# Performance work log

Hardware: AMD Instinct MI355X
Metric: run time of the kernel (lower is better)

The kernel has to match this reference:

```python
import jax, jax.numpy as jnp
import numpy as np

N = 8192      # nodes
E = 262144    # edges (avg degree 32)
D_IN = 128    # feat dim (out_channels)
D_H = 256     # hidden_channels * 2
D_OUT = 64    # in_channels (final embedding dim)


def _sage_pool(feat, src, dst, n, Wp, bp, Ws, Wn, b, ew):
    # DGL SAGEConv('pool'): h_pool = relu(fc_pool(feat)); msg = h_pool[src] * ew;
    # h_neigh = max over in-edges (0 for isolated nodes);
    # out = fc_self(feat) + fc_neigh(h_neigh) + bias
    h = jax.nn.relu(feat @ Wp + bp)                          # [N, d_in]
    msg = h[src] * ew[:, None]                               # [E, d_in]
    agg = jax.ops.segment_max(msg, dst, num_segments=n)      # [N, d_in], -inf if no in-edges
    agg = jnp.where(jnp.isfinite(agg), agg, 0.0)
    return feat @ Ws + agg @ Wn + b


def setup_inputs() -> dict:
    key = jax.random.key(0)
    ks = jax.random.split(key, 20)
    feat = jax.random.normal(ks[0], (N, D_IN), dtype=jnp.float32)
    src = jax.random.randint(ks[1], (E,), 0, N)
    dst = jax.random.randint(ks[2], (E,), 0, N)
    edge_weight = jax.random.uniform(ks[3], (E,), dtype=jnp.float32)

    def lin(k, din, dout):
        return jax.random.normal(k, (din, dout), dtype=jnp.float32) / np.float32(np.sqrt(din))

    params = {}
    dims = [(D_IN, D_H), (D_H, D_H), (D_H, D_OUT)]
    i = 4
    for l, (di, do) in enumerate(dims, 1):
        params[f"Wp{l}"] = lin(ks[i], di, di); i += 1
        params[f"bp{l}"] = jnp.zeros((di,), jnp.float32)
        params[f"Ws{l}"] = lin(ks[i], di, do); i += 1
        params[f"Wn{l}"] = lin(ks[i], di, do); i += 1
        params[f"b{l}"] = jnp.zeros((do,), jnp.float32)

    return dict(feat=feat, src=src, dst=dst, edge_weight=edge_weight, n_nodes=N, **params)


def reference(feat, src, dst, edge_weight, n_nodes,
              Wp1, bp1, Ws1, Wn1, b1,
              Wp2, bp2, Ws2, Wn2, b2,
              Wp3, bp3, Ws3, Wn3, b3):
    hd = jax.nn.relu(_sage_pool(feat, src, dst, n_nodes, Wp1, bp1, Ws1, Wn1, b1, edge_weight))
    hd = jax.nn.relu(_sage_pool(hd,   src, dst, n_nodes, Wp2, bp2, Ws2, Wn2, b2, edge_weight))
    hd = jax.nn.relu(_sage_pool(hd,   src, dst, n_nodes, Wp3, bp3, Ws3, Wn3, b3, edge_weight))
    adj_rec = hd @ hd.T                                      # [N, N]
    return hd, adj_rec
```

## Files before the change

kernel.cpp:

```cpp
#include <hip/hip_runtime.h>
#include <hip/hip_bf16.h>

#define NN 8192
#define NE 262144
#define CAP 96

typedef __attribute__((ext_vector_type(8))) __bf16 bf16x8;
typedef __attribute__((ext_vector_type(4))) float f32x4;

__device__ __forceinline__ ushort f2b(float v) {
    __hip_bfloat16 b = __float2bfloat16(v);
    return *reinterpret_cast<ushort*>(&b);
}
__device__ __forceinline__ uint pack2(float lo, float hi) {
    return (uint)f2b(lo) | ((uint)f2b(hi) << 16);
}

struct PrepArgs {
    const float* feat; ushort* featb; int* cnt;
    const float* w[9]; ushort* wt[9];
};

__global__ __launch_bounds__(256) void prep_k(PrepArgs a) {
    const int bid = blockIdx.x, tid = threadIdx.x;
    if (bid < 32) {
        a.cnt[bid * 256 + tid] = 0;
        return;
    }
    if (bid < 32 + 1024) {
        int i = ((bid - 32) * 256 + tid) * 4;
        float4 f = *(const float4*)&a.feat[i];
        uint2 o; o.x = pack2(f.x, f.y); o.y = pack2(f.z, f.w);
        *(uint2*)&a.featb[i] = o;
        return;
    }
    int id = (bid - 1056) * 256 + tid;
    if (id >= 376832) return;
    const int cum[10] = {0, 16384, 49152, 81920, 147456, 212992, 278528, 344064, 360448, 376832};
    const int KK[9] = {128, 128, 128, 256, 256, 256, 256, 256, 256};
    const int LN[9] = {7, 8, 8, 8, 8, 8, 8, 6, 6};
    int m = 0;
#pragma unroll
    for (int t = 1; t < 9; ++t) m += (id >= cum[t]);
    int local = id - cum[m];
    int K = KK[m], ln = LN[m];
    int k = local >> ln, n = local & ((1 << ln) - 1);
    a.wt[m][n * K + k] = f2b(a.w[m][local]);
}

__global__ void scatter_direct_k(const int* __restrict__ src, const int* __restrict__ dst,
                                 const float* __restrict__ ew, int* __restrict__ cnt,
                                 uint2* __restrict__ slots) {
    int e = blockIdx.x * blockDim.x + threadIdx.x;
    if (e < NE) {
        int d = dst[e];
        int p = atomicAdd(&cnt[d], 1);
        if (p < CAP) slots[(size_t)d * CAP + p] = make_uint2((uint)src[e], __float_as_uint(ew[e]));
    }
}

#define AW2 72

template <int BM, int BN, bool DUAL, bool RELU, int OUTMODE>
__global__ __launch_bounds__(256, 4) void gemm_k(
    const ushort* __restrict__ A1, const ushort* __restrict__ BT1, int K1,
    const ushort* __restrict__ A2, const ushort* __restrict__ BT2, int K2,
    const float* __restrict__ bias, float* __restrict__ Cf,
    ushort* __restrict__ Cb, int N) {
    constexpr int MI = BM / 32, NJ = BN / 32;
    __shared__ __align__(16) ushort As[BM * AW2];
    __shared__ __align__(16) ushort Bs[BN * AW2];

    int tid = threadIdx.x;
    int lane = tid & 63, wave = tid >> 6;
    int wm = (wave >> 1) * (BM / 2), wn = (wave & 1) * (BN / 2);
    int r16 = lane & 15, kb = lane >> 4;
    int m0 = blockIdx.y * BM, n0 = blockIdx.x * BN;

    f32x4 acc[MI][NJ];
#pragma unroll
    for (int i = 0; i < MI; ++i)
#pragma unroll
        for (int j = 0; j < NJ; ++j) acc[i][j] = (f32x4)(0.f);

#pragma unroll 1
    for (int pass = 0; pass < (DUAL ? 2 : 1); ++pass) {
        const ushort* A = pass ? A2 : A1;
        const ushort* BT = pass ? BT2 : BT1;
        int K = pass ? K2 : K1;
        for (int k0 = 0; k0 < K; k0 += 64) {
#pragma unroll
            for (int rep = 0; rep < BM / 32; ++rep) {
                int id = rep * 256 + tid;
                int row = id >> 3, c = id & 7;
                *(bf16x8*)&As[row * AW2 + c * 8] =
                    *(const bf16x8*)&A[(size_t)(m0 + row) * K + k0 + c * 8];
            }
#pragma unroll
            for (int rep = 0; rep < BN / 32; ++rep) {
                int id = rep * 256 + tid;
                int row = id >> 3, c = id & 7;
                *(bf16x8*)&Bs[row * AW2 + c * 8] =
                    *(const bf16x8*)&BT[(size_t)(n0 + row) * K + k0 + c * 8];
            }
            __syncthreads();
#pragma unroll
            for (int kc = 0; kc < 2; ++kc) {
                bf16x8 a[MI], b[NJ];
#pragma unroll
                for (int i = 0; i < MI; ++i)
                    a[i] = *(const bf16x8*)&As[(wm + 16 * i + r16) * AW2 + kc * 32 + kb * 8];
#pragma unroll
                for (int j = 0; j < NJ; ++j)
                    b[j] = *(const bf16x8*)&Bs[(wn + 16 * j + r16) * AW2 + kc * 32 + kb * 8];
#pragma unroll
                for (int i = 0; i < MI; ++i)
#pragma unroll
                    for (int j = 0; j < NJ; ++j)
                        acc[i][j] = __builtin_amdgcn_mfma_f32_16x16x32_bf16(a[i], b[j], acc[i][j], 0, 0, 0);
            }
            __syncthreads();
        }
    }

#pragma unroll
    for (int i = 0; i < MI; ++i) {
#pragma unroll
        for (int j = 0; j < NJ; ++j) {
            int col = n0 + wn + 16 * j + r16;
            float bv = bias[col];
#pragma unroll
            for (int r = 0; r < 4; ++r) {
                int row = m0 + wm + 16 * i + kb * 4 + r;
                float v = acc[i][j][r] + bv;
                if (RELU) v = fmaxf(v, 0.f);
                if (OUTMODE != 0) Cf[(size_t)row * N + col] = v;
                if (OUTMODE != 1) Cb[(size_t)row * N + col] = f2b(v);
            }
        }
    }
}

template <int D>
__global__ __launch_bounds__(256) void seg_max_k4(
    const ushort* __restrict__ h, const int* __restrict__ cnt,
    const uint2* __restrict__ slots, ushort* __restrict__ agg) {
    constexpr int FPL = D / 64;
    int wave = threadIdx.x >> 6, lane = threadIdx.x & 63;
    int node = blockIdx.x * 4 + wave;
    int f0 = lane * FPL;
    int n = cnt[node];
    if (n > CAP) n = CAP;
    const uint2* sl = &slots[(size_t)node * CAP];
    float mx[FPL];
#pragma unroll
    for (int i = 0; i < FPL; ++i) mx[i] = 0.f;

    auto upd = [&](uint s, float w) {
        const uint* hp = (const uint*)&h[(size_t)s * D + f0];
#pragma unroll
        for (int c = 0; c < FPL / 2; ++c) {
            uint u = hp[c];
            float lo = __uint_as_float(u << 16);
            float hi = __uint_as_float(u & 0xffff0000u);
            mx[2 * c] = fmaxf(mx[2 * c], lo * w);
            mx[2 * c + 1] = fmaxf(mx[2 * c + 1], hi * w);
        }
    };

    int e = 0;
    for (; e + 8 <= n; e += 8) {
        uint2 d[8];
#pragma unroll
        for (int t = 0; t < 8; ++t) d[t] = sl[e + t];
#pragma unroll
        for (int t = 0; t < 8; ++t) upd(d[t].x, __uint_as_float(d[t].y));
    }
    for (; e < n; ++e) {
        uint2 d = sl[e];
        upd(d.x, __uint_as_float(d.y));
    }

    uint* ap = (uint*)&agg[(size_t)node * D + f0];
#pragma unroll
    for (int c = 0; c < FPL / 2; ++c) ap[c] = pack2(mx[2 * c], mx[2 * c + 1]);
}

__global__ __launch_bounds__(256) void aat_k(const ushort* __restrict__ H,
                                             float* __restrict__ C) {
    __shared__ __align__(16) ushort As[128 * 72];
    __shared__ __align__(16) ushort Bs[128 * 72];
    int tid = threadIdx.x, lane = tid & 63, wave = tid >> 6;
    int wm = (wave >> 1) * 64, wn = (wave & 1) * 64;
    int r16 = lane & 15, kb = lane >> 4;
    int m0 = blockIdx.y * 128, n0 = blockIdx.x * 128;

#pragma unroll
    for (int rep = 0; rep < 4; ++rep) {
        int id = rep * 256 + tid;
        int row = id >> 3, c = id & 7;
        *(bf16x8*)&As[row * 72 + c * 8] = *(const bf16x8*)&H[(size_t)(m0 + row) * 64 + c * 8];
        *(bf16x8*)&Bs[row * 72 + c * 8] = *(const bf16x8*)&H[(size_t)(n0 + row) * 64 + c * 8];
    }
    __syncthreads();

    f32x4 acc[4][4];
#pragma unroll
    for (int i = 0; i < 4; ++i)
#pragma unroll
        for (int j = 0; j < 4; ++j) acc[i][j] = (f32x4)(0.f);

#pragma unroll
    for (int kc = 0; kc < 2; ++kc) {
        bf16x8 a[4], b[4];
#pragma unroll
        for (int i = 0; i < 4; ++i)
            a[i] = *(const bf16x8*)&As[(wm + 16 * i + r16) * 72 + kc * 32 + kb * 8];
#pragma unroll
        for (int j = 0; j < 4; ++j)
            b[j] = *(const bf16x8*)&Bs[(wn + 16 * j + r16) * 72 + kc * 32 + kb * 8];
#pragma unroll
        for (int i = 0; i < 4; ++i)
#pragma unroll
            for (int j = 0; j < 4; ++j)
                acc[i][j] = __builtin_amdgcn_mfma_f32_16x16x32_bf16(a[i], b[j], acc[i][j], 0, 0, 0);
    }

#pragma unroll
    for (int i = 0; i < 4; ++i) {
#pragma unroll
        for (int j = 0; j < 4; ++j) {
            int col = n0 + wn + 16 * j + r16;
#pragma unroll
            for (int r = 0; r < 4; ++r) {
                size_t row = m0 + wm + 16 * i + kb * 4 + r;
                C[row * NN + col] = acc[i][j][r];
            }
        }
    }
}

extern "C" void kernel_launch(void* const* d_in, const int* in_sizes, int n_in,
                              void* d_out, int out_size, void* d_ws, size_t ws_size,
                              hipStream_t stream) {
    const float* feat = (const float*)d_in[0];
    const int* src = (const int*)d_in[1];
    const int* dst = (const int*)d_in[2];
    const float* ew = (const float*)d_in[3];
    const float* Wp1 = (const float*)d_in[5];
    const float* bp1 = (const float*)d_in[6];
    const float* Ws1 = (const float*)d_in[7];
    const float* Wn1 = (const float*)d_in[8];
    const float* b1  = (const float*)d_in[9];
    const float* Wp2 = (const float*)d_in[10];
    const float* bp2 = (const float*)d_in[11];
    const float* Ws2 = (const float*)d_in[12];
    const float* Wn2 = (const float*)d_in[13];
    const float* b2  = (const float*)d_in[14];
    const float* Wp3 = (const float*)d_in[15];
    const float* bp3 = (const float*)d_in[16];
    const float* Ws3 = (const float*)d_in[17];
    const float* Wn3 = (const float*)d_in[18];
    const float* b3  = (const float*)d_in[19];

    float* out = (float*)d_out;
    float* adj = out + (size_t)NN * 64;

    char* ws = (char*)d_ws;
    int* cnt      = (int*)(ws + 0x0);
    uint2* slots  = (uint2*)(ws + 0x10000);
    ushort* featb = (ushort*)(ws + 0x620000);
    ushort* Wp1T = (ushort*)(ws + 0x820000);
    ushort* Ws1T = (ushort*)(ws + 0x828000);
    ushort* Wn1T = (ushort*)(ws + 0x838000);
    ushort* Wp2T = (ushort*)(ws + 0x848000);
    ushort* Ws2T = (ushort*)(ws + 0x868000);
    ushort* Wn2T = (ushort*)(ws + 0x888000);
    ushort* Wp3T = (ushort*)(ws + 0x8A8000);
    ushort* Ws3T = (ushort*)(ws + 0x8C8000);
    ushort* Wn3T = (ushort*)(ws + 0x8D0000);
    ushort* P = (ushort*)(ws + 0x900000);
    ushort* G = (ushort*)(ws + 0xD00000);
    ushort* X = (ushort*)(ws + 0x1100000);
    ushort* Y = (ushort*)(ws + 0x1500000);
    ushort* hdb = (ushort*)(ws + 0x1900000);

    PrepArgs pa;
    pa.feat = feat; pa.featb = featb; pa.cnt = cnt;
    const float* wsrc[9] = {Wp1, Ws1, Wn1, Wp2, Ws2, Wn2, Wp3, Ws3, Wn3};
    ushort* wdst[9] = {Wp1T, Ws1T, Wn1T, Wp2T, Ws2T, Wn2T, Wp3T, Ws3T, Wn3T};
    for (int i = 0; i < 9; ++i) { pa.w[i] = wsrc[i]; pa.wt[i] = wdst[i]; }
    prep_k<<<32 + 1024 + 1472, 256, 0, stream>>>(pa);

    scatter_direct_k<<<NE / 256, 256, 0, stream>>>(src, dst, ew, cnt, slots);

    gemm_k<64, 64, false, true, 0><<<dim3(2, 128), 256, 0, stream>>>(
        featb, Wp1T, 128, nullptr, nullptr, 0, bp1, nullptr, P, 128);
    seg_max_k4<128><<<NN / 4, 256, 0, stream>>>(P, cnt, slots, G);
    gemm_k<64, 64, true, true, 0><<<dim3(4, 128), 256, 0, stream>>>(
        featb, Ws1T, 128, G, Wn1T, 128, b1, nullptr, X, 256);

    gemm_k<64, 64, false, true, 0><<<dim3(4, 128), 256, 0, stream>>>(
        X, Wp2T, 256, nullptr, nullptr, 0, bp2, nullptr, P, 256);
    seg_max_k4<256><<<NN / 4, 256, 0, stream>>>(P, cnt, slots, G);
    gemm_k<64, 64, true, true, 0><<<dim3(4, 128), 256, 0, stream>>>(
        X, Ws2T, 256, G, Wn2T, 256, b2, nullptr, Y, 256);

    gemm_k<64, 64, false, true, 0><<<dim3(4, 128), 256, 0, stream>>>(
        Y, Wp3T, 256, nullptr, nullptr, 0, bp3, nullptr, P, 256);
    seg_max_k4<256><<<NN / 4, 256, 0, stream>>>(P, cnt, slots, G);
    gemm_k<32, 64, true, true, 2><<<dim3(1, 256), 256, 0, stream>>>(
        Y, Ws3T, 256, G, Wn3T, 256, b3, out, hdb, 64);

    aat_k<<<dim3(NN / 128, NN / 128), 256, 0, stream>>>(hdb, adj);
}
```

Measured before the change: 166.5 us.

## Fuse segment-max, self/neigh GEMMs and next-layer pool GEMM per layer

Replaces the separate pool GEMM, segment-max and dual GEMM launches with one per-layer kernel. Each block gathers the max-aggregated neighbour features for 32 nodes into shared memory, runs the self and neighbour GEMMs, and then computes the next layer's pool projection from the tile held in shared memory. The layer-1 pool GEMM also moves into the scatter kernel, and feat is converted to bf16 inside the GEMM loads instead of in a separate pass. This removes several launches and the global round trips of G and P, but the 32-row tiles with only 256 blocks mean lower occupancy, and the atomic scatter and pool1 blocks in one grid can run concurrently. That is a correctness risk: layer_k reads cnt and slots only in a later launch, so it is probably fine.

```diff
diff --git a/kernel.cpp b/kernel.cpp
--- a/kernel.cpp
+++ b/kernel.cpp
@@ -17,24 +17,14 @@
 }
 
 struct PrepArgs {
-    const float* feat; ushort* featb; int* cnt;
+    int* cnt;
     const float* w[9]; ushort* wt[9];
 };
 
 __global__ __launch_bounds__(256) void prep_k(PrepArgs a) {
     const int bid = blockIdx.x, tid = threadIdx.x;
-    if (bid < 32) {
-        a.cnt[bid * 256 + tid] = 0;
-        return;
-    }
-    if (bid < 32 + 1024) {
-        int i = ((bid - 32) * 256 + tid) * 4;
-        float4 f = *(const float4*)&a.feat[i];
-        uint2 o; o.x = pack2(f.x, f.y); o.y = pack2(f.z, f.w);
-        *(uint2*)&a.featb[i] = o;
-        return;
-    }
-    int id = (bid - 1056) * 256 + tid;
+    if (bid < 32) { a.cnt[bid * 256 + tid] = 0; return; }
+    int id = (bid - 32) * 256 + tid;
     if (id >= 376832) return;
     const int cum[10] = {0, 16384, 49152, 81920, 147456, 212992, 278528, 344064, 360448, 376832};
     const int KK[9] = {128, 128, 128, 256, 256, 256, 256, 256, 256};
@@ -48,142 +38,236 @@
     a.wt[m][n * K + k] = f2b(a.w[m][local]);
 }
 
-__global__ void scatter_direct_k(const int* __restrict__ src, const int* __restrict__ dst,
-                                 const float* __restrict__ ew, int* __restrict__ cnt,
-                                 uint2* __restrict__ slots) {
-    int e = blockIdx.x * blockDim.x + threadIdx.x;
-    if (e < NE) {
+__global__ __launch_bounds__(256) void scat_pool1_k(
+    const int* __restrict__ src, const int* __restrict__ dst,
+    const float* __restrict__ ew, int* __restrict__ cnt, uint2* __restrict__ slots,
+    const float* __restrict__ feat, const ushort* __restrict__ WpT,
+    const float* __restrict__ bp, ushort* __restrict__ Pout) {
+    const int tid = threadIdx.x;
+    if (blockIdx.x < NE / 256) {
+        int e = blockIdx.x * 256 + tid;
         int d = dst[e];
         int p = atomicAdd(&cnt[d], 1);
         if (p < CAP) slots[(size_t)d * CAP + p] = make_uint2((uint)src[e], __float_as_uint(ew[e]));
-    }
-}
-
-#define AW2 72
-
-template <int BM, int BN, bool DUAL, bool RELU, int OUTMODE>
-__global__ __launch_bounds__(256, 4) void gemm_k(
-    const ushort* __restrict__ A1, const ushort* __restrict__ BT1, int K1,
-    const ushort* __restrict__ A2, const ushort* __restrict__ BT2, int K2,
-    const float* __restrict__ bias, float* __restrict__ Cf,
-    ushort* __restrict__ Cb, int N) {
-    constexpr int MI = BM / 32, NJ = BN / 32;
-    __shared__ __align__(16) ushort As[BM * AW2];
-    __shared__ __align__(16) ushort Bs[BN * AW2];
-
-    int tid = threadIdx.x;
-    int lane = tid & 63, wave = tid >> 6;
-    int wm = (wave >> 1) * (BM / 2), wn = (wave & 1) * (BN / 2);
-    int r16 = lane & 15, kb = lane >> 4;
-    int m0 = blockIdx.y * BM, n0 = blockIdx.x * BN;
-
-    f32x4 acc[MI][NJ];
-#pragma unroll
-    for (int i = 0; i < MI; ++i)
-#pragma unroll
-        for (int j = 0; j < NJ; ++j) acc[i][j] = (f32x4)(0.f);
-
-#pragma unroll 1
-    for (int pass = 0; pass < (DUAL ? 2 : 1); ++pass) {
-        const ushort* A = pass ? A2 : A1;
-        const ushort* BT = pass ? BT2 : BT1;
-        int K = pass ? K2 : K1;
-        for (int k0 = 0; k0 < K; k0 += 64) {
-#pragma unroll
-            for (int rep = 0; rep < BM / 32; ++rep) {
+        return;
+    }
+    __shared__ __align__(16) ushort As[32 * 72];
+    __shared__ __align__(16) ushort Bs[128 * 72];
+    const int m0 = (blockIdx.x - NE / 256) * 32;
+    const int lane = tid & 63, wave = tid >> 6;
+    const int r16 = lane & 15, kb = lane >> 4;
+    const int wm = (wave >> 1) * 16, wn = (wave & 1) * 64;
+
+    f32x4 acc[4];
+#pragma unroll
+    for (int j = 0; j < 4; ++j) acc[j] = (f32x4)(0.f);
+
+#pragma unroll
+    for (int k0 = 0; k0 < 128; k0 += 64) {
+#pragma unroll
+        for (int rep = 0; rep < 2; ++rep) {
+            int id = rep * 256 + tid;
+            int row = id >> 4, c = id & 15;
+            float4 f = *(const float4*)&feat[(size_t)(m0 + row) * 128 + k0 + c * 4];
+            uint2 o; o.x = pack2(f.x, f.y); o.y = pack2(f.z, f.w);
+            *(uint2*)&As[row * 72 + c * 4] = o;
+        }
+#pragma unroll
+        for (int rep = 0; rep < 4; ++rep) {
+            int id = rep * 256 + tid;
+            int row = id >> 3, c = id & 7;
+            *(bf16x8*)&Bs[row * 72 + c * 8] = *(const bf16x8*)&WpT[(size_t)row * 128 + k0 + c * 8];
+        }
+        __syncthreads();
+#pragma unroll
+        for (int kc = 0; kc < 2; ++kc) {
+            bf16x8 a = *(const bf16x8*)&As[(wm + r16) * 72 + kc * 32 + kb * 8];
+#pragma unroll
+            for (int j = 0; j < 4; ++j) {
+                bf16x8 b = *(const bf16x8*)&Bs[(wn + 16 * j + r16) * 72 + kc * 32 + kb * 8];
+                acc[j] = __builtin_amdgcn_mfma_f32_16x16x32_bf16(a, b, acc[j], 0, 0, 0);
+            }
+        }
+        __syncthreads();
+    }
+#pragma unroll
+    for (int j = 0; j < 4; ++j) {
+        int col = wn + 16 * j + r16;
+        float bv = bp[col];
+#pragma unroll
+        for (int rr = 0; rr < 4; ++rr) {
+            int rl = wm + kb * 4 + rr;
+            Pout[(size_t)(m0 + rl) * 128 + col] = f2b(fmaxf(acc[j][rr] + bv, 0.f));
+        }
+    }
+}
+
+template <int DIN, int DOUT, bool A1F32, bool POOL, bool LAST>
+__global__ __launch_bounds__(256) void layer_k(
+    const void* __restrict__ A1v, const ushort* __restrict__ Pin,
+    const int* __restrict__ cnt, const uint2* __restrict__ slots,
+    const ushort* __restrict__ WsT, const ushort* __restrict__ WnT,
+    const float* __restrict__ bias,
+    const ushort* __restrict__ WpT, const float* __restrict__ biasp,
+    ushort* __restrict__ Xout, float* __restrict__ Fout, ushort* __restrict__ Pout) {
+    constexpr int SG = DIN + 8, ST = DOUT + 8, NJ = DOUT / 32, FPL = DIN / 64;
+    __shared__ __align__(16) ushort G[32 * SG];
+    __shared__ __align__(16) ushort T[32 * ST];
+    __shared__ __align__(16) ushort As[32 * 72];
+    __shared__ __align__(16) ushort Bs[DOUT * 72];
+
+    const int tid = threadIdx.x, lane = tid & 63, wave = tid >> 6;
+    const int r16 = lane & 15, kb = lane >> 4;
+    const int wm = (wave >> 1) * 16, wn = (wave & 1) * (DOUT / 2);
+    const int m0 = blockIdx.x * 32;
+
+    {
+        const int f0 = lane * FPL;
+        for (int r = 0; r < 8; ++r) {
+            int nl = wave * 8 + r, node = m0 + nl;
+            int n = cnt[node]; if (n > CAP) n = CAP;
+            const uint2* sl = &slots[(size_t)node * CAP];
+            float mx[FPL];
+#pragma unroll
+            for (int i = 0; i < FPL; ++i) mx[i] = 0.f;
+            auto upd = [&](uint s, float w) {
+                const uint* hp = (const uint*)&Pin[(size_t)s * DIN + f0];
+#pragma unroll
+                for (int c = 0; c < FPL / 2; ++c) {
+                    uint u = hp[c];
+                    float lo = __uint_as_float(u << 16);
+                    float hi = __uint_as_float(u & 0xffff0000u);
+                    mx[2 * c] = fmaxf(mx[2 * c], lo * w);
+                    mx[2 * c + 1] = fmaxf(mx[2 * c + 1], hi * w);
+                }
+            };
+            int e = 0;
+            for (; e + 8 <= n; e += 8) {
+                uint2 d[8];
+#pragma unroll
+                for (int t = 0; t < 8; ++t) d[t] = sl[e + t];
+#pragma unroll
+                for (int t = 0; t < 8; ++t) upd(d[t].x, __uint_as_float(d[t].y));
+            }
+            for (; e < n; ++e) { uint2 d = sl[e]; upd(d.x, __uint_as_float(d.y)); }
+            uint* gp = (uint*)&G[nl * SG + f0];
+#pragma unroll
+            for (int c = 0; c < FPL / 2; ++c) gp[c] = pack2(mx[2 * c], mx[2 * c + 1]);
+        }
+    }
+    __syncthreads();
+
+    f32x4 acc[NJ];
+#pragma unroll
+    for (int j = 0; j < NJ; ++j) acc[j] = (f32x4)(0.f);
+
+    for (int k0 = 0; k0 < DIN; k0 += 64) {
+        if constexpr (A1F32) {
+            const float* A1 = (const float*)A1v;
+#pragma unroll
+            for (int rep = 0; rep < 2; ++rep) {
+                int id = rep * 256 + tid;
+                int row = id >> 4, c = id & 15;
+                float4 f = *(const float4*)&A1[(size_t)(m0 + row) * DIN + k0 + c * 4];
+                uint2 o; o.x = pack2(f.x, f.y); o.y = pack2(f.z, f.w);
+                *(uint2*)&As[row * 72 + c * 4] = o;
+            }
+        } else {
+            const ushort* A1 = (const ushort*)A1v;
+            int row = tid >> 3, c = tid & 7;
+            *(bf16x8*)&As[row * 72 + c * 8] = *(const bf16x8*)&A1[(size_t)(m0 + row) * DIN + k0 + c * 8];
+        }
+#pragma unroll
+        for (int rep = 0; rep < DOUT / 32; ++rep) {
+            int id = rep * 256 + tid;
+            int row = id >> 3, c = id & 7;
+            *(bf16x8*)&Bs[row * 72 + c * 8] = *(const bf16x8*)&WsT[(size_t)row * DIN + k0 + c * 8];
+        }
+        __syncthreads();
+#pragma unroll
+        for (int kc = 0; kc < 2; ++kc) {
+            bf16x8 a = *(const bf16x8*)&As[(wm + r16) * 72 + kc * 32 + kb * 8];
+#pragma unroll
+            for (int j = 0; j < NJ; ++j) {
+                bf16x8 b = *(const bf16x8*)&Bs[(wn + 16 * j + r16) * 72 + kc * 32 + kb * 8];
+                acc[j] = __builtin_amdgcn_mfma_f32_16x16x32_bf16(a, b, acc[j], 0, 0, 0);
+            }
+        }
+        __syncthreads();
+    }
+    for (int k0 = 0; k0 < DIN; k0 += 64) {
+#pragma unroll
+        for (int rep = 0; rep < DOUT / 32; ++rep) {
+            int id = rep * 256 + tid;
+            int row = id >> 3, c = id & 7;
+            *(bf16x8*)&Bs[row * 72 + c * 8] = *(const bf16x8*)&WnT[(size_t)row * DIN + k0 + c * 8];
+        }
+        __syncthreads();
+#pragma unroll
+        for (int kc = 0; kc < 2; ++kc) {
+            bf16x8 a = *(const bf16x8*)&G[(wm + r16) * SG + k0 + kc * 32 + kb * 8];
+#pragma unroll
+            for (int j = 0; j < NJ; ++j) {
+                bf16x8 b = *(const bf16x8*)&Bs[(wn + 16 * j + r16) * 72 + kc * 32 + kb * 8];
+                acc[j] = __builtin_amdgcn_mfma_f32_16x16x32_bf16(a, b, acc[j], 0, 0, 0);
+            }
+        }
+        __syncthreads();
+    }
+
+#pragma unroll
+    for (int j = 0; j < NJ; ++j) {
+        int col = wn + 16 * j + r16;
+        float bv = bias[col];
+#pragma unroll
+        for (int rr = 0; rr < 4; ++rr) {
+            int rl = wm + kb * 4 + rr;
+            float v = fmaxf(acc[j][rr] + bv, 0.f);
+            if constexpr (LAST) {
+                Fout[(size_t)(m0 + rl) * DOUT + col] = v;
+                Xout[(size_t)(m0 + rl) * DOUT + col] = f2b(v);
+            } else {
+                T[rl * ST + col] = f2b(v);
+                Xout[(size_t)(m0 + rl) * DOUT + col] = f2b(v);
+            }
+        }
+    }
+
+    if constexpr (POOL) {
+        __syncthreads();
+        f32x4 acc2[NJ];
+#pragma unroll
+        for (int j = 0; j < NJ; ++j) acc2[j] = (f32x4)(0.f);
+        for (int k0 = 0; k0 < DOUT; k0 += 64) {
+#pragma unroll
+            for (int rep = 0; rep < DOUT / 32; ++rep) {
                 int id = rep * 256 + tid;
                 int row = id >> 3, c = id & 7;
-                *(bf16x8*)&As[row * AW2 + c * 8] =
-                    *(const bf16x8*)&A[(size_t)(m0 + row) * K + k0 + c * 8];
-            }
-#pragma unroll
-            for (int rep = 0; rep < BN / 32; ++rep) {
-                int id = rep * 256 + tid;
-                int row = id >> 3, c = id & 7;
-                *(bf16x8*)&Bs[row * AW2 + c * 8] =
-                    *(const bf16x8*)&BT[(size_t)(n0 + row) * K + k0 + c * 8];
+                *(bf16x8*)&Bs[row * 72 + c * 8] = *(const bf16x8*)&WpT[(size_t)row * DOUT + k0 + c * 8];
             }
             __syncthreads();
 #pragma unroll
             for (int kc = 0; kc < 2; ++kc) {
-                bf16x8 a[MI], b[NJ];
-#pragma unroll
-                for (int i = 0; i < MI; ++i)
-                    a[i] = *(const bf16x8*)&As[(wm + 16 * i + r16) * AW2 + kc * 32 + kb * 8];
-#pragma unroll
-                for (int j = 0; j < NJ; ++j)
-                    b[j] = *(const bf16x8*)&Bs[(wn + 16 * j + r16) * AW2 + kc * 32 + kb * 8];
-#pragma unroll
-                for (int i = 0; i < MI; ++i)
-#pragma unroll
-                    for (int j = 0; j < NJ; ++j)
-                        acc[i][j] = __builtin_amdgcn_mfma_f32_16x16x32_bf16(a[i], b[j], acc[i][j], 0, 0, 0);
+                bf16x8 a = *(const bf16x8*)&T[(wm + r16) * ST + k0 + kc * 32 + kb * 8];
+#pragma unroll
+                for (int j = 0; j < NJ; ++j) {
+                    bf16x8 b = *(const bf16x8*)&Bs[(wn + 16 * j + r16) * 72 + kc * 32 + kb * 8];
+                    acc2[j] = __builtin_amdgcn_mfma_f32_16x16x32_bf16(a, b, acc2[j], 0, 0, 0);
+                }
             }
             __syncthreads();
         }
-    }
-
-#pragma unroll
-    for (int i = 0; i < MI; ++i) {
 #pragma unroll
         for (int j = 0; j < NJ; ++j) {
-            int col = n0 + wn + 16 * j + r16;
-            float bv = bias[col];
-#pragma unroll
-            for (int r = 0; r < 4; ++r) {
-                int row = m0 + wm + 16 * i + kb * 4 + r;
-                float v = acc[i][j][r] + bv;
-                if (RELU) v = fmaxf(v, 0.f);
-                if (OUTMODE != 0) Cf[(size_t)row * N + col] = v;
-                if (OUTMODE != 1) Cb[(size_t)row * N + col] = f2b(v);
-            }
-        }
-    }
-}
-
-template <int D>
-__global__ __launch_bounds__(256) void seg_max_k4(
-    const ushort* __restrict__ h, const int* __restrict__ cnt,
-    const uint2* __restrict__ slots, ushort* __restrict__ agg) {
-    constexpr int FPL = D / 64;
-    int wave = threadIdx.x >> 6, lane = threadIdx.x & 63;
-    int node = blockIdx.x * 4 + wave;
-    int f0 = lane * FPL;
-    int n = cnt[node];
-    if (n > CAP) n = CAP;
-    const uint2* sl = &slots[(size_t)node * CAP];
-    float mx[FPL];
-#pragma unroll
-    for (int i = 0; i < FPL; ++i) mx[i] = 0.f;
-
-    auto upd = [&](uint s, float w) {
-        const uint* hp = (const uint*)&h[(size_t)s * D + f0];
-#pragma unroll
-        for (int c = 0; c < FPL / 2; ++c) {
-            uint u = hp[c];
-            float lo = __uint_as_float(u << 16);
-            float hi = __uint_as_float(u & 0xffff0000u);
-            mx[2 * c] = fmaxf(mx[2 * c], lo * w);
-            mx[2 * c + 1] = fmaxf(mx[2 * c + 1], hi * w);
-        }
-    };
-
-    int e = 0;
-    for (; e + 8 <= n; e += 8) {
-        uint2 d[8];
-#pragma unroll
-        for (int t = 0; t < 8; ++t) d[t] = sl[e + t];
-#pragma unroll
-        for (int t = 0; t < 8; ++t) upd(d[t].x, __uint_as_float(d[t].y));
-    }
-    for (; e < n; ++e) {
-        uint2 d = sl[e];
-        upd(d.x, __uint_as_float(d.y));
-    }
-
-    uint* ap = (uint*)&agg[(size_t)node * D + f0];
-#pragma unroll
-    for (int c = 0; c < FPL / 2; ++c) ap[c] = pack2(mx[2 * c], mx[2 * c + 1]);
+            int col = wn + 16 * j + r16;
+            float bv = biasp[col];
+#pragma unroll
+            for (int rr = 0; rr < 4; ++rr) {
+                int rl = wm + kb * 4 + rr;
+                Pout[(size_t)(m0 + rl) * DOUT + col] = f2b(fmaxf(acc2[j][rr] + bv, 0.f));
+            }
+        }
+    }
 }
 
 __global__ __launch_bounds__(256) void aat_k(const ushort* __restrict__ H,
@@ -269,48 +353,38 @@
     char* ws = (char*)d_ws;
     int* cnt      = (int*)(ws + 0x0);
     uint2* slots  = (uint2*)(ws + 0x10000);
-    ushort* featb = (ushort*)(ws + 0x620000);
-    ushort* Wp1T = (ushort*)(ws + 0x820000);
-    ushort* Ws1T = (ushort*)(ws + 0x828000);
-    ushort* Wn1T = (ushort*)(ws + 0x838000);
-    ushort* Wp2T = (ushort*)(ws + 0x848000);
-    ushort* Ws2T = (ushort*)(ws + 0x868000);
-    ushort* Wn2T = (ushort*)(ws + 0x888000);
-    ushort* Wp3T = (ushort*)(ws + 0x8A8000);
-    ushort* Ws3T = (ushort*)(ws + 0x8C8000);
-    ushort* Wn3T = (ushort*)(ws + 0x8D0000);
-    ushort* P = (ushort*)(ws + 0x900000);
-    ushort* G = (ushort*)(ws + 0xD00000);
-    ushort* X = (ushort*)(ws + 0x1100000);
-    ushort* Y = (ushort*)(ws + 0x1500000);
+    ushort* Wp1T = (ushort*)(ws + 0x620000);
+    ushort* Ws1T = (ushort*)(ws + 0x628000);
+    ushort* Wn1T = (ushort*)(ws + 0x638000);
+    ushort* Wp2T = (ushort*)(ws + 0x648000);
+    ushort* Ws2T = (ushort*)(ws + 0x668000);
+    ushort* Wn2T = (ushort*)(ws + 0x688000);
+    ushort* Wp3T = (ushort*)(ws + 0x6A8000);
+    ushort* Ws3T = (ushort*)(ws + 0x6C8000);
+    ushort* Wn3T = (ushort*)(ws + 0x6D0000);
+    ushort* P1 = (ushort*)(ws + 0x700000);
+    ushort* P2 = (ushort*)(ws + 0x900000);
+    ushort* P3 = (ushort*)(ws + 0xD00000);
+    ushort* X  = (ushort*)(ws + 0x1100000);
+    ushort* Y  = (ushort*)(ws + 0x1500000);
     ushort* hdb = (ushort*)(ws + 0x1900000);
 
     PrepArgs pa;
-    pa.feat = feat; pa.featb = featb; pa.cnt = cnt;
+    pa.cnt = cnt;
     const float* wsrc[9] = {Wp1, Ws1, Wn1, Wp2, Ws2, Wn2, Wp3, Ws3, Wn3};
     ushort* wdst[9] = {Wp1T, Ws1T, Wn1T, Wp2T, Ws2T, Wn2T, Wp3T, Ws3T, Wn3T};
     for (int i = 0; i < 9; ++i) { pa.w[i] = wsrc[i]; pa.wt[i] = wdst[i]; }
-    prep_k<<<32 + 1024 + 1472, 256, 0, stream>>>(pa);
-
-    scatter_direct_k<<<NE / 256, 256, 0, stream>>>(src, dst, ew, cnt, slots);
-
-    gemm_k<64, 64, false, true, 0><<<dim3(2, 128), 256, 0, stream>>>(
-        featb, Wp1T, 128, nullptr, nullptr, 0, bp1, nullptr, P, 128);
-    seg_max_k4<128><<<NN / 4, 256, 0, stream>>>(P, cnt, slots, G);
-    gemm_k<64, 64, true, true, 0><<<dim3(4, 128), 256, 0, stream>>>(
-        featb, Ws1T, 128, G, Wn1T, 128, b1, nullptr, X, 256);
-
-    gemm_k<64, 64, false, true, 0><<<dim3(4, 128), 256, 0, stream>>>(
-        X, Wp2T, 256, nullptr, nullptr, 0, bp2, nullptr, P, 256);
-    seg_max_k4<256><<<NN / 4, 256, 0, stream>>>(P, cnt, slots, G);
-    gemm_k<64, 64, true, true, 0><<<dim3(4, 128), 256, 0, stream>>>(
-        X, Ws2T, 256, G, Wn2T, 256, b2, nullptr, Y, 256);
-
-    gemm_k<64, 64, false, true, 0><<<dim3(4, 128), 256, 0, stream>>>(
-        Y, Wp3T, 256, nullptr, nullptr, 0, bp3, nullptr, P, 256);
-    seg_max_k4<256><<<NN / 4, 256, 0, stream>>>(P, cnt, slots, G);
-    gemm_k<32, 64, true, true, 2><<<dim3(1, 256), 256, 0, stream>>>(
-        Y, Ws3T, 256, G, Wn3T, 256, b3, out, hdb, 64);
+    prep_k<<<32 + 1472, 256, 0, stream>>>(pa);
+
+    scat_pool1_k<<<NE / 256 + NN / 32, 256, 0, stream>>>(
+        src, dst, ew, cnt, slots, feat, Wp1T, bp1, P1);
+
+    layer_k<128, 256, true, true, false><<<NN / 32, 256, 0, stream>>>(
+        feat, P1, cnt, slots, Ws1T, Wn1T, b1, Wp2T, bp2, X, nullptr, P2);
+    layer_k<256, 256, false, true, false><<<NN / 32, 256, 0, stream>>>(
+        X, P2, cnt, slots, Ws2T, Wn2T, b2, Wp3T, bp3, Y, nullptr, P3);
+    layer_k<256, 64, false, false, true><<<NN / 32, 256, 0, stream>>>(
+        Y, P3, cnt, slots, Ws3T, Wn3T, b3, nullptr, nullptr, hdb, out, nullptr);
 
     aat_k<<<dim3(NN / 128, NN / 128), 256, 0, stream>>>(hdb, adj);
 }
```

Result: slower. 204.6 us (+22.9%).

## Co-schedule self-GEMM with segment max and fold scatter into prep

Applied to the files above, without the earlier changes.

The fc_self GEMM now runs inside the same launch as the segment-max gather, on extra blocks, and writes a bf16 partial. The neighbour GEMM then adds that partial instead of running a dual-pass GEMM. The edge scatter is merged into the weight-prep kernel, with the counter reset done by a memset. The fp32-to-bf16 conversion of feat moves into the first GEMM's tile loads, and the GEMM K-tile grows from 64 to 128. This aims to overlap memory-bound gathers with MFMA work and cut launches, at the cost of an extra bf16 rounding of the self term and an extra intermediate round trip.

```diff
diff --git a/kernel.cpp b/kernel.cpp
--- a/kernel.cpp
+++ b/kernel.cpp
@@ -15,26 +15,26 @@
 __device__ __forceinline__ uint pack2(float lo, float hi) {
     return (uint)f2b(lo) | ((uint)f2b(hi) << 16);
 }
+__device__ __forceinline__ float b2f(ushort u) {
+    return __uint_as_float(((uint)u) << 16);
+}
 
 struct PrepArgs {
-    const float* feat; ushort* featb; int* cnt;
+    const int* src; const int* dst; const float* ew;
+    int* cnt; uint2* slots;
     const float* w[9]; ushort* wt[9];
 };
 
-__global__ __launch_bounds__(256) void prep_k(PrepArgs a) {
+__global__ __launch_bounds__(256) void prep_scatter_k(PrepArgs a) {
     const int bid = blockIdx.x, tid = threadIdx.x;
-    if (bid < 32) {
-        a.cnt[bid * 256 + tid] = 0;
+    if (bid < 1024) {
+        int e = bid * 256 + tid;
+        int d = a.dst[e];
+        int p = atomicAdd(&a.cnt[d], 1);
+        if (p < CAP) a.slots[(size_t)d * CAP + p] = make_uint2((uint)a.src[e], __float_as_uint(a.ew[e]));
         return;
     }
-    if (bid < 32 + 1024) {
-        int i = ((bid - 32) * 256 + tid) * 4;
-        float4 f = *(const float4*)&a.feat[i];
-        uint2 o; o.x = pack2(f.x, f.y); o.y = pack2(f.z, f.w);
-        *(uint2*)&a.featb[i] = o;
-        return;
-    }
-    int id = (bid - 1056) * 256 + tid;
+    int id = (bid - 1024) * 256 + tid;
     if (id >= 376832) return;
     const int cum[10] = {0, 16384, 49152, 81920, 147456, 212992, 278528, 344064, 360448, 376832};
     const int KK[9] = {128, 128, 128, 256, 256, 256, 256, 256, 256};
@@ -48,34 +48,21 @@
     a.wt[m][n * K + k] = f2b(a.w[m][local]);
 }
 
-__global__ void scatter_direct_k(const int* __restrict__ src, const int* __restrict__ dst,
-                                 const float* __restrict__ ew, int* __restrict__ cnt,
-                                 uint2* __restrict__ slots) {
-    int e = blockIdx.x * blockDim.x + threadIdx.x;
-    if (e < NE) {
-        int d = dst[e];
-        int p = atomicAdd(&cnt[d], 1);
-        if (p < CAP) slots[(size_t)d * CAP + p] = make_uint2((uint)src[e], __float_as_uint(ew[e]));
-    }
-}
-
-#define AW2 72
-
-template <int BM, int BN, bool DUAL, bool RELU, int OUTMODE>
+#define AWK 136
+
+template <int BM, int BN, bool A1F32, bool RELU, int OUTMODE, bool ADDC>
 __global__ __launch_bounds__(256, 4) void gemm_k(
-    const ushort* __restrict__ A1, const ushort* __restrict__ BT1, int K1,
-    const ushort* __restrict__ A2, const ushort* __restrict__ BT2, int K2,
-    const float* __restrict__ bias, float* __restrict__ Cf,
-    ushort* __restrict__ Cb, int N) {
+    const void* __restrict__ Av, const ushort* __restrict__ BT, int K,
+    const float* __restrict__ bias, const ushort* __restrict__ cin,
+    float* __restrict__ Cf, ushort* __restrict__ Cb, int N) {
     constexpr int MI = BM / 32, NJ = BN / 32;
-    __shared__ __align__(16) ushort As[BM * AW2];
-    __shared__ __align__(16) ushort Bs[BN * AW2];
-
-    int tid = threadIdx.x;
-    int lane = tid & 63, wave = tid >> 6;
-    int wm = (wave >> 1) * (BM / 2), wn = (wave & 1) * (BN / 2);
-    int r16 = lane & 15, kb = lane >> 4;
-    int m0 = blockIdx.y * BM, n0 = blockIdx.x * BN;
+    __shared__ __align__(16) ushort As[BM * AWK];
+    __shared__ __align__(16) ushort Bs[BN * AWK];
+
+    const int tid = threadIdx.x, lane = tid & 63, wave = tid >> 6;
+    const int wm = (wave >> 1) * (BM / 2), wn = (wave & 1) * (BN / 2);
+    const int r16 = lane & 15, kb = lane >> 4;
+    const int m0 = blockIdx.y * BM, n0 = blockIdx.x * BN;
 
     f32x4 acc[MI][NJ];
 #pragma unroll
@@ -83,44 +70,178 @@
 #pragma unroll
         for (int j = 0; j < NJ; ++j) acc[i][j] = (f32x4)(0.f);
 
-#pragma unroll 1
-    for (int pass = 0; pass < (DUAL ? 2 : 1); ++pass) {
-        const ushort* A = pass ? A2 : A1;
-        const ushort* BT = pass ? BT2 : BT1;
-        int K = pass ? K2 : K1;
-        for (int k0 = 0; k0 < K; k0 += 64) {
-#pragma unroll
-            for (int rep = 0; rep < BM / 32; ++rep) {
+    for (int k0 = 0; k0 < K; k0 += 128) {
+        if constexpr (A1F32) {
+            const float* A = (const float*)Av;
+#pragma unroll
+            for (int rep = 0; rep < BM / 8; ++rep) {
                 int id = rep * 256 + tid;
-                int row = id >> 3, c = id & 7;
-                *(bf16x8*)&As[row * AW2 + c * 8] =
+                int row = id >> 5, c = id & 31;
+                float4 f = *(const float4*)&A[(size_t)(m0 + row) * K + k0 + c * 4];
+                uint2 o; o.x = pack2(f.x, f.y); o.y = pack2(f.z, f.w);
+                *(uint2*)&As[row * AWK + c * 4] = o;
+            }
+        } else {
+            const ushort* A = (const ushort*)Av;
+#pragma unroll
+            for (int rep = 0; rep < BM / 16; ++rep) {
+                int id = rep * 256 + tid;
+                int row = id >> 4, c = id & 15;
+                *(bf16x8*)&As[row * AWK + c * 8] =
                     *(const bf16x8*)&A[(size_t)(m0 + row) * K + k0 + c * 8];
             }
-#pragma unroll
-            for (int rep = 0; rep < BN / 32; ++rep) {
+        }
+#pragma unroll
+        for (int rep = 0; rep < BN / 16; ++rep) {
+            int id = rep * 256 + tid;
+            int row = id >> 4, c = id & 15;
+            *(bf16x8*)&Bs[row * AWK + c * 8] =
+                *(const bf16x8*)&BT[(size_t)(n0 + row) * K + k0 + c * 8];
+        }
+        __syncthreads();
+#pragma unroll
+        for (int kc = 0; kc < 4; ++kc) {
+            bf16x8 a[MI], b[NJ];
+#pragma unroll
+            for (int i = 0; i < MI; ++i)
+                a[i] = *(const bf16x8*)&As[(wm + 16 * i + r16) * AWK + kc * 32 + kb * 8];
+#pragma unroll
+            for (int j = 0; j < NJ; ++j)
+                b[j] = *(const bf16x8*)&Bs[(wn + 16 * j + r16) * AWK + kc * 32 + kb * 8];
+#pragma unroll
+            for (int i = 0; i < MI; ++i)
+#pragma unroll
+                for (int j = 0; j < NJ; ++j)
+                    acc[i][j] = __builtin_amdgcn_mfma_f32_16x16x32_bf16(a[i], b[j], acc[i][j], 0, 0, 0);
+        }
+        __syncthreads();
+    }
+
+#pragma unroll
+    for (int i = 0; i < MI; ++i) {
+#pragma unroll
+        for (int j = 0; j < NJ; ++j) {
+            int col = n0 + wn + 16 * j + r16;
+            float bv = ADDC ? 0.f : bias[col];
+#pragma unroll
+            for (int r = 0; r < 4; ++r) {
+                int row = m0 + wm + 16 * i + kb * 4 + r;
+                float v = acc[i][j][r];
+                if constexpr (ADDC) v += b2f(cin[(size_t)row * N + col]);
+                else v += bv;
+                if (RELU) v = fmaxf(v, 0.f);
+                if (OUTMODE != 0) Cf[(size_t)row * N + col] = v;
+                if (OUTMODE != 1) Cb[(size_t)row * N + col] = f2b(v);
+            }
+        }
+    }
+}
+
+template <int DIN, int DOUT, bool A1F32>
+__global__ __launch_bounds__(256, 4) void seg_self_k(
+    const ushort* __restrict__ Pin, const int* __restrict__ cnt,
+    const uint2* __restrict__ slots, ushort* __restrict__ G,
+    const void* __restrict__ Av, const ushort* __restrict__ WsT,
+    const float* __restrict__ bias, ushort* __restrict__ Cself) {
+    constexpr int BM = (DOUT == 64) ? 32 : 64;
+    constexpr int NBX = DOUT / 64;
+    constexpr int MI = BM / 32, NJ = 2;
+    __shared__ __align__(16) ushort As[BM * AWK];
+    __shared__ __align__(16) ushort Bs[64 * AWK];
+
+    const int tid = threadIdx.x, lane = tid & 63, wave = tid >> 6;
+
+    if (blockIdx.x < 2048) {
+        constexpr int FPL = DIN / 64;
+        int node = blockIdx.x * 4 + wave;
+        int f0 = lane * FPL;
+        int n = cnt[node]; if (n > CAP) n = CAP;
+        const uint2* sl = &slots[(size_t)node * CAP];
+        float mx[FPL];
+#pragma unroll
+        for (int i = 0; i < FPL; ++i) mx[i] = 0.f;
+        auto upd = [&](uint s, float w) {
+            const uint* hp = (const uint*)&Pin[(size_t)s * DIN + f0];
+#pragma unroll
+            for (int c = 0; c < FPL / 2; ++c) {
+                uint u = hp[c];
+                float lo = __uint_as_float(u << 16);
+                float hi = __uint_as_float(u & 0xffff0000u);
+                mx[2 * c] = fmaxf(mx[2 * c], lo * w);
+                mx[2 * c + 1] = fmaxf(mx[2 * c + 1], hi * w);
+            }
+        };
+        int e = 0;
+        for (; e + 8 <= n; e += 8) {
+            uint2 d[8];
+#pragma unroll
+            for (int t = 0; t < 8; ++t) d[t] = sl[e + t];
+#pragma unroll
+            for (int t = 0; t < 8; ++t) upd(d[t].x, __uint_as_float(d[t].y));
+        }
+        for (; e < n; ++e) { uint2 d = sl[e]; upd(d.x, __uint_as_float(d.y)); }
+        uint* gp = (uint*)&G[(size_t)node * DIN + f0];
+#pragma unroll
+        for (int c = 0; c < FPL / 2; ++c) gp[c] = pack2(mx[2 * c], mx[2 * c + 1]);
+        return;
+    }
+
+    const int bx = blockIdx.x - 2048;
+    const int n0 = (bx % NBX) * 64, m0 = (bx / NBX) * BM;
+    const int wm = (wave >> 1) * (BM / 2), wn = (wave & 1) * 32;
+    const int r16 = lane & 15, kb = lane >> 4;
+
+    f32x4 acc[MI][NJ];
+#pragma unroll
+    for (int i = 0; i < MI; ++i)
+#pragma unroll
+        for (int j = 0; j < NJ; ++j) acc[i][j] = (f32x4)(0.f);
+
+    for (int k0 = 0; k0 < DIN; k0 += 128) {
+        if constexpr (A1F32) {
+            const float* A = (const float*)Av;
+#pragma unroll
+            for (int rep = 0; rep < BM / 8; ++rep) {
                 int id = rep * 256 + tid;
-                int row = id >> 3, c = id & 7;
-                *(bf16x8*)&Bs[row * AW2 + c * 8] =
-                    *(const bf16x8*)&BT[(size_t)(n0 + row) * K + k0 + c * 8];
-            }
-            __syncthreads();
-#pragma unroll
-            for (int kc = 0; kc < 2; ++kc) {
-                bf16x8 a[MI], b[NJ];
-#pragma unroll
-                for (int i = 0; i < MI; ++i)
-                    a[i] = *(const bf16x8*)&As[(wm + 16 * i + r16) * AW2 + kc * 32 + kb * 8];
+                int row = id >> 5, c = id & 31;
+                float4 f = *(const float4*)&A[(size_t)(m0 + row) * DIN + k0 + c * 4];
+                uint2 o; o.x = pack2(f.x, f.y); o.y = pack2(f.z, f.w);
+                *(uint2*)&As[row * AWK + c * 4] = o;
+            }
+        } else {
+            const ushort* A = (const ushort*)Av;
+#pragma unroll
+            for (int rep = 0; rep < BM / 16; ++rep) {
+                int id = rep * 256 + tid;
+                int row = id >> 4, c = id & 15;
+                *(bf16x8*)&As[row * AWK + c * 8] =
+                    *(const bf16x8*)&A[(size_t)(m0 + row) * DIN + k0 + c * 8];
+            }
+        }
+#pragma unroll
+        for (int rep = 0; rep < 4; ++rep) {
+            int id = rep * 256 + tid;
+            int row = id >> 4, c = id & 15;
+            *(bf16x8*)&Bs[row * AWK + c * 8] =
+                *(const bf16x8*)&WsT[(size_t)(n0 + row) * DIN + k0 + c * 8];
+        }
+        __syncthreads();
+#pragma unroll
+        for (int kc = 0; kc < 4; ++kc) {
+            bf16x8 a[MI], b[NJ];
+#pragma unroll
+            for (int i = 0; i < MI; ++i)
+                a[i] = *(const bf16x8*)&As[(wm + 16 * i + r16) * AWK + kc * 32 + kb * 8];
+#pragma unroll
+            for (int j = 0; j < NJ; ++j)
+                b[j] = *(const bf16x8*)&Bs[(wn + 16 * j + r16) * AWK + kc * 32 + kb * 8];
+#pragma unroll
+            for (int i = 0; i < MI; ++i)
 #pragma unroll
                 for (int j = 0; j < NJ; ++j)
-                    b[j] = *(const bf16x8*)&Bs[(wn + 16 * j + r16) * AW2 + kc * 32 + kb * 8];
-#pragma unroll
-                for (int i = 0; i < MI; ++i)
-#pragma unroll
-                    for (int j = 0; j < NJ; ++j)
-                        acc[i][j] = __builtin_amdgcn_mfma_f32_16x16x32_bf16(a[i], b[j], acc[i][j], 0, 0, 0);
-            }
-            __syncthreads();
-        }
+                    acc[i][j] = __builtin_amdgcn_mfma_f32_16x16x32_bf16(a[i], b[j], acc[i][j], 0, 0, 0);
+        }
+        __syncthreads();
     }
 
 #pragma unroll
@@ -132,58 +253,10 @@
 #pragma unroll
             for (int r = 0; r < 4; ++r) {
                 int row = m0 + wm + 16 * i + kb * 4 + r;
-                float v = acc[i][j][r] + bv;
-                if (RELU) v = fmaxf(v, 0.f);
-                if (OUTMODE != 0) Cf[(size_t)row * N + col] = v;
-                if (OUTMODE != 1) Cb[(size_t)row * N + col] = f2b(v);
-            }
-        }
-    }
-}
-
-template <int D>
-__global__ __launch_bounds__(256) void seg_max_k4(
-    const ushort* __restrict__ h, const int* __restrict__ cnt,
-    const uint2* __restrict__ slots, ushort* __restrict__ agg) {
-    constexpr int FPL = D / 64;
-    int wave = threadIdx.x >> 6, lane = threadIdx.x & 63;
-    int node = blockIdx.x * 4 + wave;
-    int f0 = lane * FPL;
-    int n = cnt[node];
-    if (n > CAP) n = CAP;
-    const uint2* sl = &slots[(size_t)node * CAP];
-    float mx[FPL];
-#pragma unroll
-    for (int i = 0; i < FPL; ++i) mx[i] = 0.f;
-
-    auto upd = [&](uint s, float w) {
-        const uint* hp = (const uint*)&h[(size_t)s * D + f0];
-#pragma unroll
-        for (int c = 0; c < FPL / 2; ++c) {
-            uint u = hp[c];
-            float lo = __uint_as_float(u << 16);
-            float hi = __uint_as_float(u & 0xffff0000u);
-            mx[2 * c] = fmaxf(mx[2 * c], lo * w);
-            mx[2 * c + 1] = fmaxf(mx[2 * c + 1], hi * w);
-        }
-    };
-
-    int e = 0;
-    for (; e + 8 <= n; e += 8) {
-        uint2 d[8];
-#pragma unroll
-        for (int t = 0; t < 8; ++t) d[t] = sl[e + t];
-#pragma unroll
-        for (int t = 0; t < 8; ++t) upd(d[t].x, __uint_as_float(d[t].y));
-    }
-    for (; e < n; ++e) {
-        uint2 d = sl[e];
-        upd(d.x, __uint_as_float(d.y));
-    }
-
-    uint* ap = (uint*)&agg[(size_t)node * D + f0];
-#pragma unroll
-    for (int c = 0; c < FPL / 2; ++c) ap[c] = pack2(mx[2 * c], mx[2 * c + 1]);
+                Cself[(size_t)row * DOUT + col] = f2b(acc[i][j][r] + bv);
+            }
+        }
+    }
 }
 
 __global__ __launch_bounds__(256) void aat_k(const ushort* __restrict__ H,
@@ -269,48 +342,51 @@
     char* ws = (char*)d_ws;
     int* cnt      = (int*)(ws + 0x0);
     uint2* slots  = (uint2*)(ws + 0x10000);
-    ushort* featb = (ushort*)(ws + 0x620000);
-    ushort* Wp1T = (ushort*)(ws + 0x820000);
-    ushort* Ws1T = (ushort*)(ws + 0x828000);
-    ushort* Wn1T = (ushort*)(ws + 0x838000);
-    ushort* Wp2T = (ushort*)(ws + 0x848000);
-    ushort* Ws2T = (ushort*)(ws + 0x868000);
-    ushort* Wn2T = (ushort*)(ws + 0x888000);
-    ushort* Wp3T = (ushort*)(ws + 0x8A8000);
-    ushort* Ws3T = (ushort*)(ws + 0x8C8000);
-    ushort* Wn3T = (ushort*)(ws + 0x8D0000);
-    ushort* P = (ushort*)(ws + 0x900000);
-    ushort* G = (ushort*)(ws + 0xD00000);
-    ushort* X = (ushort*)(ws + 0x1100000);
-    ushort* Y = (ushort*)(ws + 0x1500000);
-    ushort* hdb = (ushort*)(ws + 0x1900000);
+    ushort* Wp1T = (ushort*)(ws + 0x620000);
+    ushort* Ws1T = (ushort*)(ws + 0x628000);
+    ushort* Wn1T = (ushort*)(ws + 0x638000);
+    ushort* Wp2T = (ushort*)(ws + 0x648000);
+    ushort* Ws2T = (ushort*)(ws + 0x668000);
+    ushort* Wn2T = (ushort*)(ws + 0x688000);
+    ushort* Wp3T = (ushort*)(ws + 0x6A8000);
+    ushort* Ws3T = (ushort*)(ws + 0x6C8000);
+    ushort* Wn3T = (ushort*)(ws + 0x6D0000);
+    ushort* P  = (ushort*)(ws + 0x700000);
+    ushort* G  = (ushort*)(ws + 0xB00000);
+    ushort* X  = (ushort*)(ws + 0xF00000);
+    ushort* Y  = (ushort*)(ws + 0x1300000);
+    ushort* Cs = (ushort*)(ws + 0x1700000);
+    ushort* hdb = (ushort*)(ws + 0x1B00000);
+
+    hipMemsetAsync(cnt, 0, NN * sizeof(int), stream);
 
     PrepArgs pa;
-    pa.feat = feat; pa.featb = featb; pa.cnt = cnt;
+    pa.src = src; pa.dst = dst; pa.ew = ew; pa.cnt = cnt; pa.slots = slots;
     const float* wsrc[9] = {Wp1, Ws1, Wn1, Wp2, Ws2, Wn2, Wp3, Ws3, Wn3};
     ushort* wdst[9] = {Wp1T, Ws1T, Wn1T, Wp2T, Ws2T, Wn2T, Wp3T, Ws3T, Wn3T};
     for (int i = 0; i < 9; ++i) { pa.w[i] = wsrc[i]; pa.wt[i] = wdst[i]; }
-    prep_k<<<32 + 1024 + 1472, 256, 0, stream>>>(pa);
-
-    scatter_direct_k<<<NE / 256, 256, 0, stream>>>(src, dst, ew, cnt, slots);
-
-    gemm_k<64, 64, false, true, 0><<<dim3(2, 128), 256, 0, stream>>>(
-        featb, Wp1T, 128, nullptr, nullptr, 0, bp1, nullptr, P, 128);
-    seg_max_k4<128><<<NN / 4, 256, 0, stream>>>(P, cnt, slots, G);
-    gemm_k<64, 64, true, true, 0><<<dim3(4, 128), 256, 0, stream>>>(
-        featb, Ws1T, 128, G, Wn1T, 128, b1, nullptr, X, 256);
-
-    gemm_k<64, 64, false, true, 0><<<dim3(4, 128), 256, 0, stream>>>(
-        X, Wp2T, 256, nullptr, nullptr, 0, bp2, nullptr, P, 256);
-    seg_max_k4<256><<<NN / 4, 256, 0, stream>>>(P, cnt, slots, G);
-    gemm_k<64, 64, true, true, 0><<<dim3(4, 128), 256, 0, stream>>>(
-        X, Ws2T, 256, G, Wn2T, 256, b2, nullptr, Y, 256);
-
-    gemm_k<64, 64, false, true, 0><<<dim3(4, 128), 256, 0, stream>>>(
-        Y, Wp3T, 256, nullptr, nullptr, 0, bp3, nullptr, P, 256);
-    seg_max_k4<256><<<NN / 4, 256, 0, stream>>>(P, cnt, slots, G);
-    gemm_k<32, 64, true, true, 2><<<dim3(1, 256), 256, 0, stream>>>(
-        Y, Ws3T, 256, G, Wn3T, 256, b3, out, hdb, 64);
+    prep_scatter_k<<<1024 + 1472, 256, 0, stream>>>(pa);
+
+    gemm_k<64, 64, true, true, 0, false><<<dim3(2, 128), 256, 0, stream>>>(
+        feat, Wp1T, 128, bp1, nullptr, nullptr, P, 128);
+    seg_self_k<128, 256, true><<<2048 + 512, 256, 0, stream>>>(
+        P, cnt, slots, G, feat, Ws1T, b1, Cs);
+    gemm_k<64, 64, false, true, 0, true><<<dim3(4, 128), 256, 0, stream>>>(
+        G, Wn1T, 128, nullptr, Cs, nullptr, X, 256);
+
+    gemm_k<64, 64, false, true, 0, false><<<dim3(4, 128), 256, 0, stream>>>(
+        X, Wp2T, 256, bp2, nullptr, nullptr, P, 256);
+    seg_self_k<256, 256, false><<<2048 + 512, 256, 0, stream>>>(
+        P, cnt, slots, G, X, Ws2T, b2, Cs);
+    gemm_k<64, 64, false, true, 0, true><<<dim3(4, 128), 256, 0, stream>>>(
+        G, Wn2T, 256, nullptr, Cs, nullptr, Y, 256);
+
+    gemm_k<64, 64, false, true, 0, false><<<dim3(4, 128), 256, 0, stream>>>(
+        Y, Wp3T, 256, bp3, nullptr, nullptr, P, 256);
+    seg_self_k<256, 64, false><<<2048 + 256, 256, 0, stream>>>(
+        P, cnt, slots, G, Y, Ws3T, b3, Cs);
+    gemm_k<32, 64, false, true, 2, true><<<dim3(1, 256), 256, 0, stream>>>(
+        G, Wn3T, 256, nullptr, Cs, out, hdb, 64);
 
     aat_k<<<dim3(NN / 128, NN / 128), 256, 0, stream>>>(hdb, adj);
 }
```

New measurement: 165.3 us. Within noise of the previous version (-0.7%).
